# Optimization experiments

Measured on AMD Instinct MI355X. Metric: run time of the kernel, lower is better.

The kernel has to match this reference:

```python
import jax, jax.numpy as jnp
import numpy as np

N_NODES = 100000
N_EDGES = 1600000
N_FEAT = 128
HIDDEN = 64
N_LAYERS = 3


def setup_inputs() -> dict:
    key = jax.random.key(0)
    ks = jax.random.split(key, 8)
    x = jax.random.normal(ks[0], (N_NODES, N_FEAT), dtype=jnp.float32)
    edge_index = jax.random.randint(ks[1], (2, N_EDGES), 0, N_NODES, dtype=jnp.int64)
    s_emb = 1.0 / np.sqrt(N_FEAT)
    s_h = 1.0 / np.sqrt(HIDDEN)
    W_emb = jax.random.uniform(ks[2], (N_FEAT, HIDDEN), jnp.float32, -s_emb, s_emb)
    b_emb = jax.random.uniform(ks[3], (HIDDEN,), jnp.float32, -s_emb, s_emb)
    Ws = jax.random.uniform(ks[4], (N_LAYERS, HIDDEN, HIDDEN), jnp.float32, -s_h, s_h)
    bs = jax.random.uniform(ks[5], (N_LAYERS, HIDDEN), jnp.float32, -s_h, s_h)
    return {"x": x, "edge_index": edge_index, "W_emb": W_emb, "b_emb": b_emb,
            "Ws": Ws, "bs": bs}


def gcn_conv(h, src, dst, W, b, deg_inv_sqrt):
    # GCNConv with self-loops and symmetric normalization (PyG semantics):
    # out_i = sum_{j->i} d_i^{-1/2} d_j^{-1/2} (h_j W) + d_i^{-1} (h_i W) + b
    hw = h @ W                                   # [N, H]
    norm = deg_inv_sqrt[src] * deg_inv_sqrt[dst]  # [E]
    msg = hw[src] * norm[:, None]                 # [E, H] gather
    agg = jax.ops.segment_sum(msg, dst, num_segments=N_NODES)  # scatter-add
    agg = agg + hw * (deg_inv_sqrt * deg_inv_sqrt)[:, None]    # self-loop term
    return agg + b


def reference(x, edge_index, W_emb, b_emb, Ws, bs):
    src, dst = edge_index[0], edge_index[1]
    # degree with self-loops (edge weight 1), shared by every layer
    deg = jnp.zeros((N_NODES,), x.dtype).at[dst].add(1.0) + 1.0
    deg_inv_sqrt = jax.lax.rsqrt(deg)

    h = x @ W_emb + b_emb  # embedding Linear
    for i in range(N_LAYERS):
        h = jax.nn.relu(gcn_conv(h, src, dst, Ws[i], bs[i], deg_inv_sqrt))
    return h
```

## Files before the change

### kernel.cpp

```cpp
#include <hip/hip_runtime.h>
#include <hip/hip_fp16.h>
#include <math.h>

#define NN 100000
#define NE 1600000
#define NF 128
#define NH 64
#define NBUCK 196
#define CHA 8192
#define CAP 10240

__global__ __launch_bounds__(256) void part_bucket2(const int* __restrict__ src,
                                                    const int* __restrict__ dst,
                                                    int* __restrict__ bcnt,
                                                    int* __restrict__ tmp, int E) {
    __shared__ int hist[NBUCK];
    __shared__ int base[NBUCK];
    int t = threadIdx.x;
    int e0 = blockIdx.x * CHA;
    int e1 = min(e0 + CHA, E);
    if (t < NBUCK) hist[t] = 0;
    __syncthreads();
    for (int i = e0 + t; i < e1; i += 256) {
        atomicAdd(&hist[dst[i] >> 9], 1);
    }
    __syncthreads();
    if (t < NBUCK) {
        int h = hist[t];
        base[t] = h ? atomicAdd(&bcnt[t], h) : 0;
        hist[t] = 0;
    }
    __syncthreads();
    for (int i = e0 + t; i < e1; i += 256) {
        int d = dst[i];
        int b = d >> 9;
        int r = atomicAdd(&hist[b], 1);
        tmp[b * CAP + base[b] + r] = ((d & 511) << 17) | src[i];
    }
}

__global__ __launch_bounds__(256) void scan_buckets(const int* __restrict__ bcnt,
                                                    int* __restrict__ cbase,
                                                    int* __restrict__ rowptr) {
    __shared__ int s[256];
    int t = threadIdx.x;
    s[t] = (t < NBUCK) ? bcnt[t] : 0;
    __syncthreads();
    for (int off = 1; off < 256; off <<= 1) {
        int v = (t >= off) ? s[t - off] : 0;
        __syncthreads();
        s[t] += v;
        __syncthreads();
    }
    if (t < NBUCK) cbase[t] = (t == 0) ? 0 : s[t - 1];
    if (t == 0) rowptr[NN] = NE;
}

__global__ __launch_bounds__(256) void bucket_finalize(const int* __restrict__ bcnt,
                                                       const int* __restrict__ cbase,
                                                       const int* __restrict__ tmp,
                                                       int* __restrict__ rowptr,
                                                       float* __restrict__ dsq,
                                                       int* __restrict__ csr_src) {
    __shared__ int ebuf[CAP];
    __shared__ int hcnt[512];
    __shared__ int hoff[512];
    __shared__ int s[256];
    int b = blockIdx.x, t = threadIdx.x;
    int cb = bcnt[b];
    int base = cbase[b];
    const int* tsrc = tmp + b * CAP;
    for (int i = t; i < cb; i += 256) ebuf[i] = tsrc[i];
    hcnt[t] = 0;
    hcnt[t + 256] = 0;
    __syncthreads();
    for (int i = t; i < cb; i += 256) atomicAdd(&hcnt[ebuf[i] >> 17], 1);
    __syncthreads();
    int c0 = hcnt[2 * t], c1 = hcnt[2 * t + 1];
    s[t] = c0 + c1;
    __syncthreads();
    for (int off = 1; off < 256; off <<= 1) {
        int v = (t >= off) ? s[t - off] : 0;
        __syncthreads();
        s[t] += v;
        __syncthreads();
    }
    int pb = (t == 0) ? 0 : s[t - 1];
    hoff[2 * t] = pb;
    hoff[2 * t + 1] = pb + c0;
    __syncthreads();
    int nodelo = b << 9;
    int nnodes = min(512, NN - nodelo);
    for (int i = t; i < nnodes; i += 256) {
        rowptr[nodelo + i] = base + hoff[i];
        dsq[nodelo + i] = rsqrtf((float)hcnt[i] + 1.0f);
    }
    __syncthreads();
    for (int i = t; i < cb; i += 256) {
        int e = ebuf[i];
        int dlow = e >> 17;
        int p = atomicAdd(&hoff[dlow], 1);
        csr_src[base + p] = e & 0x1FFFF;
    }
}

__global__ __launch_bounds__(256) void combine_w(const float* __restrict__ We,
                                                 const float* __restrict__ be,
                                                 const float* __restrict__ W0,
                                                 float* __restrict__ Wc,
                                                 float* __restrict__ bc) {
    __shared__ float w0[NH * NH];
    int t = threadIdx.x;
    for (int i = t; i < NH * NH; i += 256) w0[i] = W0[i];
    __syncthreads();
    int row = blockIdx.x * 4 + (t >> 6);
    int col = t & 63;
    float a = 0.f;
#pragma unroll 8
    for (int k = 0; k < NH; ++k) a += We[row * NH + k] * w0[k * NH + col];
    Wc[row * NH + col] = a;
    if (blockIdx.x == 0 && t < NH) {
        float s = 0.f;
        for (int k = 0; k < NH; ++k) s += be[k] * w0[k * NH + t];
        bc[t] = s;
    }
}

__global__ __launch_bounds__(256) void fuse0_gemm(const float* __restrict__ x,
                                                  const float* __restrict__ Wc,
                                                  const float* __restrict__ bc,
                                                  const float* __restrict__ dsq,
                                                  __half* __restrict__ hws) {
    __shared__ float tile[16 * NF];
    __shared__ float red[4][16][NH];
    int t = threadIdx.x;
    int lane = t & 63;
    int wave = __builtin_amdgcn_readfirstlane(t >> 6);
    int row0 = blockIdx.x * 16;

    const float4* xsrc = (const float4*)(x + (size_t)row0 * NF);
    float4* t4 = (float4*)tile;
    t4[t] = xsrc[t];
    t4[t + 256] = xsrc[t + 256];

    float Wreg[32];
#pragma unroll
    for (int kk = 0; kk < 32; ++kk) Wreg[kk] = Wc[(wave * 32 + kk) * NH + lane];
    __syncthreads();

    float acc[16];
#pragma unroll
    for (int r = 0; r < 16; ++r) {
        const float4* rp = (const float4*)(tile + r * NF + wave * 32);
        float a = 0.f;
#pragma unroll
        for (int q = 0; q < 8; ++q) {
            float4 v = rp[q];
            a += v.x * Wreg[q * 4 + 0];
            a += v.y * Wreg[q * 4 + 1];
            a += v.z * Wreg[q * 4 + 2];
            a += v.w * Wreg[q * 4 + 3];
        }
        acc[r] = a;
    }
#pragma unroll
    for (int r = 0; r < 16; ++r) red[wave][r][lane] = acc[r];
    __syncthreads();
#pragma unroll
    for (int i = 0; i < 4; ++i) {
        int o = i * 256 + t;
        int r = o >> 6, c = o & 63;
        float s = red[0][r][c] + red[1][r][c] + red[2][r][c] + red[3][r][c];
        int row = row0 + r;
        hws[(size_t)row * NH + c] = __float2half((s + bc[c]) * dsq[row]);
    }
}

__global__ __launch_bounds__(256) void layer_gemm(const __half* __restrict__ h,
                                                  const float* __restrict__ W,
                                                  const float* __restrict__ dsq,
                                                  __half* __restrict__ hws) {
    __shared__ float tile[16 * NH];
    __shared__ float red[4][16][NH];
    int t = threadIdx.x;
    int lane = t & 63;
    int wave = __builtin_amdgcn_readfirstlane(t >> 6);
    int row0 = blockIdx.x * 16;

    {
        uint2 v = ((const uint2*)(h + (size_t)row0 * NH))[t];
        float2 p0 = __half22float2(*(const __half2*)&v.x);
        float2 p1 = __half22float2(*(const __half2*)&v.y);
        float4 f = make_float4(p0.x, p0.y, p1.x, p1.y);
        *(float4*)&tile[t * 4] = f;
    }

    float Wreg[16];
#pragma unroll
    for (int kk = 0; kk < 16; ++kk) Wreg[kk] = W[(wave * 16 + kk) * NH + lane];
    __syncthreads();

    float acc[16];
#pragma unroll
    for (int r = 0; r < 16; ++r) {
        const float4* rp = (const float4*)(tile + r * NH + wave * 16);
        float a = 0.f;
#pragma unroll
        for (int q = 0; q < 4; ++q) {
            float4 v = rp[q];
            a += v.x * Wreg[q * 4 + 0];
            a += v.y * Wreg[q * 4 + 1];
            a += v.z * Wreg[q * 4 + 2];
            a += v.w * Wreg[q * 4 + 3];
        }
        acc[r] = a;
    }
#pragma unroll
    for (int r = 0; r < 16; ++r) red[wave][r][lane] = acc[r];
    __syncthreads();
#pragma unroll
    for (int i = 0; i < 4; ++i) {
        int o = i * 256 + t;
        int r = o >> 6, c = o & 63;
        float s = red[0][r][c] + red[1][r][c] + red[2][r][c] + red[3][r][c];
        int row = row0 + r;
        hws[(size_t)row * NH + c] = __float2half(s * dsq[row]);
    }
}

#define ADDROWM(sidx, m)                                                     \
    {                                                                        \
        uint4 rv = *(const uint4*)(hws_in + (size_t)(sidx) * NH + fl);       \
        float2 f0 = __half22float2(*(const __half2*)&rv.x);                  \
        float2 f1 = __half22float2(*(const __half2*)&rv.y);                  \
        float2 f2 = __half22float2(*(const __half2*)&rv.z);                  \
        float2 f3 = __half22float2(*(const __half2*)&rv.w);                  \
        a0 += f0.x * (m); a1 += f0.y * (m); a2 += f1.x * (m); a3 += f1.y * (m); \
        a4 += f2.x * (m); a5 += f2.y * (m); a6 += f3.x * (m); a7 += f3.y * (m); \
    }

#define GATHER_BODY                                                          \
    int t = threadIdx.x;                                                     \
    int node = blockIdx.x * 4 + (t >> 6);                                    \
    int lane = t & 63;                                                       \
    int g = lane >> 3;                                                       \
    int fl = (lane & 7) << 3;                                                \
    int beg = rowptr[node], end = rowptr[node + 1];                          \
    int deg = end - beg;                                                     \
    float a0 = 0.f, a1 = 0.f, a2 = 0.f, a3 = 0.f;                            \
    float a4 = 0.f, a5 = 0.f, a6 = 0.f, a7 = 0.f;                            \
    if (g == 0) ADDROWM(node, 1.f);                                          \
    int idxl = csr_src[min(beg + lane, NE - 1)];                             \
    _Pragma("unroll")                                                        \
    for (int k = 0; k < 8; ++k) {                                            \
        if (k * 8 < deg) {                                                   \
            int e = k * 8 + g;                                               \
            int s_ = __shfl(idxl, min(e, deg - 1));                          \
            float m = (e < deg) ? 1.f : 0.f;                                 \
            ADDROWM(s_, m);                                                  \
        }                                                                    \
    }                                                                        \
    for (int jb = beg + 64; jb < end; jb += 64) {       \
        int rem = end - jb;                                                  \
        int idx2 = csr_src[min(jb + lane, NE - 1)];                          \
        _Pragma("unroll")                                                    \
        for (int k = 0; k < 8; ++k) {                                        \
            if (k * 8 < rem) {                                               \
                int e = k * 8 + g;                                           \
                int s_ = __shfl(idx2, min(e, rem - 1));                      \
                float m = (e < rem) ? 1.f : 0.f;                             \
                ADDROWM(s_, m);                                              \
            }                                                                \
        }                                                                    \
    }                                                                        \
    a0 += __shfl_xor(a0, 8);  a1 += __shfl_xor(a1, 8);                       \
    a2 += __shfl_xor(a2, 8);  a3 += __shfl_xor(a3, 8);                       \
    a4 += __shfl_xor(a4, 8);  a5 += __shfl_xor(a5, 8);                       \
    a6 += __shfl_xor(a6, 8);  a7 += __shfl_xor(a7, 8);                       \
    a0 += __shfl_xor(a0, 16); a1 += __shfl_xor(a1, 16);                      \
    a2 += __shfl_xor(a2, 16); a3 += __shfl_xor(a3, 16);                      \
    a4 += __shfl_xor(a4, 16); a5 += __shfl_xor(a5, 16);                      \
    a6 += __shfl_xor(a6, 16); a7 += __shfl_xor(a7, 16);                      \
    a0 += __shfl_xor(a0, 32); a1 += __shfl_xor(a1, 32);                      \
    a2 += __shfl_xor(a2, 32); a3 += __shfl_xor(a3, 32);                      \
    a4 += __shfl_xor(a4, 32); a5 += __shfl_xor(a5, 32);                      \
    a6 += __shfl_xor(a6, 32); a7 += __shfl_xor(a7, 32);

__global__ __launch_bounds__(256) void gather_h(const int* __restrict__ rowptr,
                                                const int* __restrict__ csr_src,
                                                const __half* __restrict__ hws_in,
                                                const float* __restrict__ dsq,
                                                const float* __restrict__ b,
                                                __half* __restrict__ hout) {
    GATHER_BODY
    if (lane < 8) {
        float ds = dsq[node];
        float4 b0 = *(const float4*)(b + fl);
        float4 b1 = *(const float4*)(b + fl + 4);
        __half2 o[4];
        o[0] = __floats2half2_rn(fmaxf(ds * a0 + b0.x, 0.f), fmaxf(ds * a1 + b0.y, 0.f));
        o[1] = __floats2half2_rn(fmaxf(ds * a2 + b0.z, 0.f), fmaxf(ds * a3 + b0.w, 0.f));
        o[2] = __floats2half2_rn(fmaxf(ds * a4 + b1.x, 0.f), fmaxf(ds * a5 + b1.y, 0.f));
        o[3] = __floats2half2_rn(fmaxf(ds * a6 + b1.z, 0.f), fmaxf(ds * a7 + b1.w, 0.f));
        *(uint4*)(hout + (size_t)node * NH + fl) = *(const uint4*)o;
    }
}

__global__ __launch_bounds__(256) void gather_out(const int* __restrict__ rowptr,
                                                  const int* __restrict__ csr_src,
                                                  const __half* __restrict__ hws_in,
                                                  const float* __restrict__ dsq,
                                                  const float* __restrict__ b,
                                                  float* __restrict__ outbuf) {
    GATHER_BODY
    if (lane < 8) {
        float ds = dsq[node];
        float4 b0 = *(const float4*)(b + fl);
        float4 b1 = *(const float4*)(b + fl + 4);
        float4 o0, o1;
        o0.x = fmaxf(ds * a0 + b0.x, 0.f);
        o0.y = fmaxf(ds * a1 + b0.y, 0.f);
        o0.z = fmaxf(ds * a2 + b0.z, 0.f);
        o0.w = fmaxf(ds * a3 + b0.w, 0.f);
        o1.x = fmaxf(ds * a4 + b1.x, 0.f);
        o1.y = fmaxf(ds * a5 + b1.y, 0.f);
        o1.z = fmaxf(ds * a6 + b1.z, 0.f);
        o1.w = fmaxf(ds * a7 + b1.w, 0.f);
        *(float4*)(outbuf + (size_t)node * NH + fl) = o0;
        *(float4*)(outbuf + (size_t)node * NH + fl + 4) = o1;
    }
}

extern "C" void kernel_launch(void* const* d_in, const int* in_sizes, int n_in,
                              void* d_out, int out_size, void* d_ws, size_t ws_size,
                              hipStream_t stream) {
    const float* x     = (const float*)d_in[0];
    const int*   ei    = (const int*)d_in[1];
    const float* W_emb = (const float*)d_in[2];
    const float* b_emb = (const float*)d_in[3];
    const float* Ws    = (const float*)d_in[4];
    const float* bs    = (const float*)d_in[5];
    float* out = (float*)d_out;

    const int* src = ei;
    const int* dst = ei + NE;

    char* w = (char*)d_ws;
    int*    bcnt     = (int*)w;               w += 256 * 4;
    int*    cbase    = (int*)w;               w += 256 * 4;
    int*    rowptr   = (int*)w;               w += (NN + 1) * 4;
    float*  dsq      = (float*)w;             w += NN * 4;
    float*  Wc       = (float*)w;             w += NF * NH * 4;
    float*  bc       = (float*)w;             w += NH * 4;
    int*    csr_src  = (int*)w;               w += NE * 4;
    int*    tmp      = (int*)w;               w += (size_t)NBUCK * CAP * 4;
    __half* Bh       = (__half*)w;            w += (size_t)NN * NH * 2;
    __half* H16      = (__half*)w;

    hipMemsetAsync(bcnt, 0, 256 * 4, stream);
    part_bucket2<<<(NE + CHA - 1) / CHA, 256, 0, stream>>>(src, dst, bcnt, tmp, NE);
    scan_buckets<<<1, 256, 0, stream>>>(bcnt, cbase, rowptr);
    bucket_finalize<<<NBUCK, 256, 0, stream>>>(bcnt, cbase, tmp, rowptr, dsq, csr_src);

    combine_w<<<NF / 4, 256, 0, stream>>>(W_emb, b_emb, Ws, Wc, bc);

    fuse0_gemm<<<NN / 16, 256, 0, stream>>>(x, Wc, bc, dsq, Bh);

    gather_h<<<NN / 4, 256, 0, stream>>>(rowptr, csr_src, Bh, dsq, bs, H16);
    layer_gemm<<<NN / 16, 256, 0, stream>>>(H16, Ws + 1 * NH * NH, dsq, Bh);
    gather_h<<<NN / 4, 256, 0, stream>>>(rowptr, csr_src, Bh, dsq, bs + NH, H16);
    layer_gemm<<<NN / 16, 256, 0, stream>>>(H16, Ws + 2 * NH * NH, dsq, Bh);
    gather_out<<<NN / 4, 256, 0, stream>>>(rowptr, csr_src, Bh, dsq,
                                           bs + 2 * NH, out);
}
```

Measured before the change: 296.4 us.

## Use fp16 MFMA for the embedding and layer GEMMs with swizzled LDS tiles

Replaces the scalar FP32 FMA GEMMs in fuse0_gemm and layer_gemm with the 16x16x32 f16 MFMA intrinsic. Each block now handles 64 rows instead of 16. Weights are pre-transposed and cast to fp16 by combine_w and a new wconv kernel, and the activation tiles are staged in XOR-swizzled LDS to avoid bank conflicts. This removes the cross-wave LDS reduction and the FP32 ALU cost. The trade-off is that x and the weights are rounded to fp16 before multiplication, and two extra small kernel launches are added.

```diff
diff --git a/kernel.cpp b/kernel.cpp
--- a/kernel.cpp
+++ b/kernel.cpp
@@ -9,6 +9,10 @@
 #define NBUCK 196
 #define CHA 8192
 #define CAP 10240
+#define NBLK 1563
+
+typedef _Float16 f16x8 __attribute__((ext_vector_type(8)));
+typedef float f32x4 __attribute__((ext_vector_type(4)));
 
 __global__ __launch_bounds__(256) void part_bucket2(const int* __restrict__ src,
                                                     const int* __restrict__ dst,
@@ -107,7 +111,7 @@
 __global__ __launch_bounds__(256) void combine_w(const float* __restrict__ We,
                                                  const float* __restrict__ be,
                                                  const float* __restrict__ W0,
-                                                 float* __restrict__ Wc,
+                                                 _Float16* __restrict__ Wct,
                                                  float* __restrict__ bc) {
     __shared__ float w0[NH * NH];
     int t = threadIdx.x;
@@ -118,7 +122,7 @@
     float a = 0.f;
 #pragma unroll 8
     for (int k = 0; k < NH; ++k) a += We[row * NH + k] * w0[k * NH + col];
-    Wc[row * NH + col] = a;
+    Wct[col * NF + row] = (_Float16)a;
     if (blockIdx.x == 0 && t < NH) {
         float s = 0.f;
         for (int k = 0; k < NH; ++k) s += be[k] * w0[k * NH + t];
@@ -126,105 +130,130 @@
     }
 }
 
+__global__ __launch_bounds__(256) void wconv(const float* __restrict__ W,
+                                             _Float16* __restrict__ Wt) {
+    int i = blockIdx.x * 256 + threadIdx.x;
+    int k = i >> 6, c = i & 63;
+    Wt[c * NH + k] = (_Float16)W[i];
+}
+
 __global__ __launch_bounds__(256) void fuse0_gemm(const float* __restrict__ x,
-                                                  const float* __restrict__ Wc,
+                                                  const _Float16* __restrict__ Wct,
                                                   const float* __restrict__ bc,
                                                   const float* __restrict__ dsq,
                                                   __half* __restrict__ hws) {
-    __shared__ float tile[16 * NF];
-    __shared__ float red[4][16][NH];
+    __shared__ _Float16 sh[64 * NF];
     int t = threadIdx.x;
     int lane = t & 63;
-    int wave = __builtin_amdgcn_readfirstlane(t >> 6);
-    int row0 = blockIdx.x * 16;
-
-    const float4* xsrc = (const float4*)(x + (size_t)row0 * NF);
-    float4* t4 = (float4*)tile;
-    t4[t] = xsrc[t];
-    t4[t + 256] = xsrc[t + 256];
-
-    float Wreg[32];
-#pragma unroll
-    for (int kk = 0; kk < 32; ++kk) Wreg[kk] = Wc[(wave * 32 + kk) * NH + lane];
-    __syncthreads();
-
-    float acc[16];
-#pragma unroll
-    for (int r = 0; r < 16; ++r) {
-        const float4* rp = (const float4*)(tile + r * NF + wave * 32);
-        float a = 0.f;
-#pragma unroll
-        for (int q = 0; q < 8; ++q) {
-            float4 v = rp[q];
-            a += v.x * Wreg[q * 4 + 0];
-            a += v.y * Wreg[q * 4 + 1];
-            a += v.z * Wreg[q * 4 + 2];
-            a += v.w * Wreg[q * 4 + 3];
+    int w = t >> 6;
+    int row0 = blockIdx.x * 64;
+
+    f16x8 bf[4][4];
+#pragma unroll
+    for (int ct = 0; ct < 4; ++ct)
+#pragma unroll
+        for (int ks = 0; ks < 4; ++ks) {
+            int col = ct * 16 + (lane & 15);
+            int k = ks * 32 + (lane >> 4) * 8;
+            bf[ct][ks] = *(const f16x8*)(Wct + col * NF + k);
         }
-        acc[r] = a;
-    }
-#pragma unroll
-    for (int r = 0; r < 16; ++r) red[wave][r][lane] = acc[r];
-    __syncthreads();
-#pragma unroll
-    for (int i = 0; i < 4; ++i) {
-        int o = i * 256 + t;
-        int r = o >> 6, c = o & 63;
-        float s = red[0][r][c] + red[1][r][c] + red[2][r][c] + red[3][r][c];
-        int row = row0 + r;
-        hws[(size_t)row * NH + c] = __float2half((s + bc[c]) * dsq[row]);
+
+    const float4* xs = (const float4*)x;
+#pragma unroll
+    for (int i = 0; i < 8; ++i) {
+        int f = t + i * 256;
+        int r = f >> 5;
+        int c4 = f & 31;
+        int row = min(row0 + r, NN - 1);
+        float4 v = xs[(size_t)row * 32 + c4];
+        __half2 h0 = __floats2half2_rn(v.x, v.y);
+        __half2 h1 = __floats2half2_rn(v.z, v.w);
+        uint2 u;
+        u.x = *(unsigned*)&h0;
+        u.y = *(unsigned*)&h1;
+        int byte = (r * 256 + c4 * 8) ^ ((r & 7) << 4);
+        *(uint2*)((char*)sh + byte) = u;
+    }
+    __syncthreads();
+
+    f32x4 acc[4] = {{0.f, 0.f, 0.f, 0.f}, {0.f, 0.f, 0.f, 0.f},
+                    {0.f, 0.f, 0.f, 0.f}, {0.f, 0.f, 0.f, 0.f}};
+    int ar = w * 16 + (lane & 15);
+    int ak = (lane >> 4) * 8;
+#pragma unroll
+    for (int ks = 0; ks < 4; ++ks) {
+        int byte = (ar * 256 + (ks * 32 + ak) * 2) ^ ((ar & 7) << 4);
+        f16x8 af = *(const f16x8*)((const char*)sh + byte);
+#pragma unroll
+        for (int ct = 0; ct < 4; ++ct)
+            acc[ct] = __builtin_amdgcn_mfma_f32_16x16x32_f16(af, bf[ct][ks], acc[ct], 0, 0, 0);
+    }
+#pragma unroll
+    for (int ct = 0; ct < 4; ++ct) {
+        int col = ct * 16 + (lane & 15);
+        float bcv = bc[col];
+#pragma unroll
+        for (int r2 = 0; r2 < 4; ++r2) {
+            int row = row0 + w * 16 + (lane >> 4) * 4 + r2;
+            if (row < NN)
+                hws[(size_t)row * NH + col] = __float2half((acc[ct][r2] + bcv) * dsq[row]);
+        }
     }
 }
 
 __global__ __launch_bounds__(256) void layer_gemm(const __half* __restrict__ h,
-                                                  const float* __restrict__ W,
+                                                  const _Float16* __restrict__ Wt,
                                                   const float* __restrict__ dsq,
                                                   __half* __restrict__ hws) {
-    __shared__ float tile[16 * NH];
-    __shared__ float red[4][16][NH];
+    __shared__ _Float16 sh[64 * NH];
     int t = threadIdx.x;
     int lane = t & 63;
-    int wave = __builtin_amdgcn_readfirstlane(t >> 6);
-    int row0 = blockIdx.x * 16;
-
-    {
-        uint2 v = ((const uint2*)(h + (size_t)row0 * NH))[t];
-        float2 p0 = __half22float2(*(const __half2*)&v.x);
-        float2 p1 = __half22float2(*(const __half2*)&v.y);
-        float4 f = make_float4(p0.x, p0.y, p1.x, p1.y);
-        *(float4*)&tile[t * 4] = f;
-    }
-
-    float Wreg[16];
-#pragma unroll
-    for (int kk = 0; kk < 16; ++kk) Wreg[kk] = W[(wave * 16 + kk) * NH + lane];
-    __syncthreads();
-
-    float acc[16];
-#pragma unroll
-    for (int r = 0; r < 16; ++r) {
-        const float4* rp = (const float4*)(tile + r * NH + wave * 16);
-        float a = 0.f;
-#pragma unroll
-        for (int q = 0; q < 4; ++q) {
-            float4 v = rp[q];
-            a += v.x * Wreg[q * 4 + 0];
-            a += v.y * Wreg[q * 4 + 1];
-            a += v.z * Wreg[q * 4 + 2];
-            a += v.w * Wreg[q * 4 + 3];
+    int w = t >> 6;
+    int row0 = blockIdx.x * 64;
+
+    f16x8 bf[4][2];
+#pragma unroll
+    for (int ct = 0; ct < 4; ++ct)
+#pragma unroll
+        for (int ks = 0; ks < 2; ++ks) {
+            int col = ct * 16 + (lane & 15);
+            int k = ks * 32 + (lane >> 4) * 8;
+            bf[ct][ks] = *(const f16x8*)(Wt + col * NH + k);
         }
-        acc[r] = a;
-    }
-#pragma unroll
-    for (int r = 0; r < 16; ++r) red[wave][r][lane] = acc[r];
-    __syncthreads();
-#pragma unroll
-    for (int i = 0; i < 4; ++i) {
-        int o = i * 256 + t;
-        int r = o >> 6, c = o & 63;
-        float s = red[0][r][c] + red[1][r][c] + red[2][r][c] + red[3][r][c];
-        int row = row0 + r;
-        hws[(size_t)row * NH + c] = __float2half(s * dsq[row]);
+
+#pragma unroll
+    for (int i = 0; i < 2; ++i) {
+        int u = t + i * 256;
+        int r = u >> 3;
+        int c8 = u & 7;
+        int row = min(row0 + r, NN - 1);
+        uint4 v = *(const uint4*)(h + (size_t)row * NH + c8 * 8);
+        int byte = (r * 128 + c8 * 16) ^ ((r & 7) << 4);
+        *(uint4*)((char*)sh + byte) = v;
+    }
+    __syncthreads();
+
+    f32x4 acc[4] = {{0.f, 0.f, 0.f, 0.f}, {0.f, 0.f, 0.f, 0.f},
+                    {0.f, 0.f, 0.f, 0.f}, {0.f, 0.f, 0.f, 0.f}};
+    int ar = w * 16 + (lane & 15);
+    int ak = (lane >> 4) * 8;
+#pragma unroll
+    for (int ks = 0; ks < 2; ++ks) {
+        int byte = (ar * 128 + (ks * 32 + ak) * 2) ^ ((ar & 7) << 4);
+        f16x8 af = *(const f16x8*)((const char*)sh + byte);
+#pragma unroll
+        for (int ct = 0; ct < 4; ++ct)
+            acc[ct] = __builtin_amdgcn_mfma_f32_16x16x32_f16(af, bf[ct][ks], acc[ct], 0, 0, 0);
+    }
+#pragma unroll
+    for (int ct = 0; ct < 4; ++ct) {
+        int col = ct * 16 + (lane & 15);
+#pragma unroll
+        for (int r2 = 0; r2 < 4; ++r2) {
+            int row = row0 + w * 16 + (lane >> 4) * 4 + r2;
+            if (row < NN)
+                hws[(size_t)row * NH + col] = __float2half(acc[ct][r2] * dsq[row]);
+        }
     }
 }
 
@@ -346,30 +375,34 @@
     const int* dst = ei + NE;
 
     char* w = (char*)d_ws;
-    int*    bcnt     = (int*)w;               w += 256 * 4;
-    int*    cbase    = (int*)w;               w += 256 * 4;
-    int*    rowptr   = (int*)w;               w += (NN + 1) * 4;
-    float*  dsq      = (float*)w;             w += NN * 4;
-    float*  Wc       = (float*)w;             w += NF * NH * 4;
-    float*  bc       = (float*)w;             w += NH * 4;
-    int*    csr_src  = (int*)w;               w += NE * 4;
-    int*    tmp      = (int*)w;               w += (size_t)NBUCK * CAP * 4;
-    __half* Bh       = (__half*)w;            w += (size_t)NN * NH * 2;
-    __half* H16      = (__half*)w;
+    int*      bcnt    = (int*)w;              w += 256 * 4;
+    int*      cbase   = (int*)w;              w += 256 * 4;
+    int*      rowptr  = (int*)w;              w += (NN + 1) * 4;
+    float*    dsq     = (float*)w;            w += NN * 4;
+    float*    bc      = (float*)w;            w += NH * 4;
+    _Float16* Wct     = (_Float16*)w;         w += NF * NH * 2;
+    _Float16* Wt1     = (_Float16*)w;         w += NH * NH * 2;
+    _Float16* Wt2     = (_Float16*)w;         w += NH * NH * 2;
+    int*      csr_src = (int*)w;              w += NE * 4;
+    int*      tmp     = (int*)w;              w += (size_t)NBUCK * CAP * 4;
+    __half*   Bh      = (__half*)w;           w += (size_t)NN * NH * 2;
+    __half*   H16     = (__half*)w;
 
     hipMemsetAsync(bcnt, 0, 256 * 4, stream);
     part_bucket2<<<(NE + CHA - 1) / CHA, 256, 0, stream>>>(src, dst, bcnt, tmp, NE);
     scan_buckets<<<1, 256, 0, stream>>>(bcnt, cbase, rowptr);
     bucket_finalize<<<NBUCK, 256, 0, stream>>>(bcnt, cbase, tmp, rowptr, dsq, csr_src);
 
-    combine_w<<<NF / 4, 256, 0, stream>>>(W_emb, b_emb, Ws, Wc, bc);
-
-    fuse0_gemm<<<NN / 16, 256, 0, stream>>>(x, Wc, bc, dsq, Bh);
+    combine_w<<<NF / 4, 256, 0, stream>>>(W_emb, b_emb, Ws, Wct, bc);
+    wconv<<<16, 256, 0, stream>>>(Ws + 1 * NH * NH, Wt1);
+    wconv<<<16, 256, 0, stream>>>(Ws + 2 * NH * NH, Wt2);
+
+    fuse0_gemm<<<NBLK, 256, 0, stream>>>(x, Wct, bc, dsq, Bh);
 
     gather_h<<<NN / 4, 256, 0, stream>>>(rowptr, csr_src, Bh, dsq, bs, H16);
-    layer_gemm<<<NN / 16, 256, 0, stream>>>(H16, Ws + 1 * NH * NH, dsq, Bh);
+    layer_gemm<<<NBLK, 256, 0, stream>>>(H16, Wt1, dsq, Bh);
     gather_h<<<NN / 4, 256, 0, stream>>>(rowptr, csr_src, Bh, dsq, bs + NH, H16);
-    layer_gemm<<<NN / 16, 256, 0, stream>>>(H16, Ws + 2 * NH * NH, dsq, Bh);
+    layer_gemm<<<NBLK, 256, 0, stream>>>(H16, Wt2, dsq, Bh);
     gather_out<<<NN / 4, 256, 0, stream>>>(rowptr, csr_src, Bh, dsq,
                                            bs + 2 * NH, out);
 }
```

New measurement: 280.7 us. 5.3% less time.
